# Performance work log

Measured on AMD Instinct MI355X. Metric: run time of the kernel, lower is better.

## Reference

```python
import math
import jax, jax.numpy as jnp
import numpy as np

B, N, DQ, DK, DV, H = 8, 1024, 256, 256, 256, 8
EPS_SM = 1e-15
EPS_LN = 1e-5


def _layer_norm(x, g, b):
    mu = jnp.mean(x, axis=-1, keepdims=True)
    var = jnp.mean((x - mu) ** 2, axis=-1, keepdims=True)
    return (x - mu) * jax.lax.rsqrt(var + EPS_LN) * g + b


def setup_inputs() -> dict:
    key = jax.random.key(0)
    ks = jax.random.split(key, 16)
    s = 0.05
    inp = {
        "Q": jax.random.normal(ks[0], (B, N, DQ), jnp.float32),
        "K": jax.random.normal(ks[1], (B, N, DK), jnp.float32),
        "lengths": jnp.clip(jax.random.randint(ks[2], (B,), 0, N), 1, N),
        "Wq": jax.random.normal(ks[3], (DQ, DV), jnp.float32) * s,
        "bq": jnp.zeros((DV,), jnp.float32),
        "Wk": jax.random.normal(ks[4], (DK, DV), jnp.float32) * s,
        "bk": jnp.zeros((DV,), jnp.float32),
        "Wv": jax.random.normal(ks[5], (DK, DV), jnp.float32) * s,
        "bv": jnp.zeros((DV,), jnp.float32),
        "Wo": jax.random.normal(ks[6], (DV, DV), jnp.float32) * s,
        "bo": jnp.zeros((DV,), jnp.float32),
        "g0": jnp.ones((DV,), jnp.float32),
        "b0": jnp.zeros((DV,), jnp.float32),
        "g1": jnp.ones((DV,), jnp.float32),
        "b1": jnp.zeros((DV,), jnp.float32),
    }
    return inp


def reference(Q, K, lengths, Wq, bq, Wk, bk, Wv, bv, Wo, bo, g0, b0, g1, b1):
    d = DV // H  # head dim
    mask = (jnp.arange(N) < lengths[:, None]).astype(Q.dtype)  # (B, N)
    q = (Q @ Wq + bq) * mask[..., None]  # (B, N, DV)
    k = (K @ Wk + bk) * mask[..., None]
    v = (K @ Wv + bv) * mask[..., None]
    qh = q.reshape(B, N, H, d)
    kh = k.reshape(B, N, H, d)
    vh = v.reshape(B, N, H, d)
    # NB: original scales by sqrt(dim_V), not sqrt(head_dim)
    scores = jnp.einsum("bnhd,bmhd->bhnm", qh, kh) / math.sqrt(DV)
    # set_softmax: raw exp, mask rows and cols by lengths, normalize over keys
    e = jnp.exp(scores) * mask[:, None, :, None] * mask[:, None, None, :]
    A = e / (jnp.sum(e, axis=-1, keepdims=True) + EPS_SM)  # (B, H, N, N)
    O = qh + jnp.einsum("bhnm,bmhd->bnhd", A, vh)  # residual per head
    O = O.reshape(B, N, DV)
    O = _layer_norm(O, g0, b0)
    O = O + jax.nn.relu(O @ Wo + bo)
    O = _layer_norm(O, g1, b1)
    return O
```

## Files before the change

kernel.cpp:

```cpp
#include <hip/hip_runtime.h>
#include <hip/hip_bf16.h>


typedef __attribute__((ext_vector_type(8))) short short8;
typedef __attribute__((ext_vector_type(4))) short short4v;
typedef __attribute__((ext_vector_type(4))) float f32x4;

__device__ __forceinline__ short f2bf(float f) {
    union { float f; unsigned u; } x; x.f = f;
    unsigned r = x.u + 0x7fffu + ((x.u >> 16) & 1u);
    return (short)(r >> 16);
}
__device__ __forceinline__ float bf2f(short s) {
    union { unsigned u; float f; } x; x.u = ((unsigned)(unsigned short)s) << 16;
    return x.f;
}

__global__ __launch_bounds__(256) void wtrans_kernel(
    const float* __restrict__ Wq, const float* __restrict__ Wk,
    const float* __restrict__ Wv, const float* __restrict__ Wo,
    short* __restrict__ WqT, short* __restrict__ WkT,
    short* __restrict__ WvT, short* __restrict__ WoT)
{
    __shared__ short tile[64][72];
    const float* W; short* T;
    switch (blockIdx.y) {
        case 0:  W = Wq; T = WqT; break;
        case 1:  W = Wk; T = WkT; break;
        case 2:  W = Wv; T = WvT; break;
        default: W = Wo; T = WoT; break;
    }
    const int k0 = (blockIdx.x >> 2) * 64;
    const int n0 = (blockIdx.x & 3) * 64;
    const int c  = threadIdx.x & 63;
    const int r4 = threadIdx.x >> 6;
    #pragma unroll
    for (int i = 0; i < 16; i++) {
        int k = r4 + i * 4;
        tile[k][c] = f2bf(W[(size_t)(k0 + k) * 256 + n0 + c]);
    }
    __syncthreads();
    #pragma unroll
    for (int i = 0; i < 16; i++) {
        int n = r4 + i * 4;
        T[(size_t)(n0 + n) * 256 + k0 + c] = tile[c][n];
    }
}

__global__ __launch_bounds__(256) void proj_kernel(
    const float* __restrict__ Q, const float* __restrict__ Kin,
    const short* __restrict__ WqT, const short* __restrict__ WkT, const short* __restrict__ WvT,
    const float* __restrict__ bq, const float* __restrict__ bk, const float* __restrict__ bv,
    const int* __restrict__ lengths,
    short* __restrict__ qb, short* __restrict__ kb, short* __restrict__ vT)
{
    __shared__ short Xt[32][264];
    const int which = blockIdx.y;
    const float* A   = (which == 0) ? Q   : Kin;
    const short* WTa = (which == 0) ? WqT : WkT;

    const int tid = threadIdx.x;
    const int b = blockIdx.x >> 5;
    const int len = lengths[b];
    const int r0b = blockIdx.x * 32;
    const int ntok0b = r0b & 1023;

    if (ntok0b < len) {
        #pragma unroll
        for (int it = 0; it < 8; it++) {
            int e = tid + it * 256;
            int row = e >> 6, c4 = (e & 63) * 4;
            float4 f = *(const float4*)(A + (size_t)(r0b + row) * 256 + c4);
            short4v s4;
            s4[0] = f2bf(f.x); s4[1] = f2bf(f.y); s4[2] = f2bf(f.z); s4[3] = f2bf(f.w);
            *(short4v*)(&Xt[row][c4]) = s4;
        }
    }
    __syncthreads();

    const int lane = tid & 63, wid = tid >> 6;
    const int m = lane & 15, quad = lane >> 4;
    const int rh = wid >> 1, ch = wid & 1;
    const int c0 = ch * 128;
    const int ntok0 = ntok0b + rh * 16;

    f32x4 accA[8], accB[8];
    #pragma unroll
    for (int t = 0; t < 8; t++) {
        accA[t] = (f32x4){0.f, 0.f, 0.f, 0.f};
        accB[t] = (f32x4){0.f, 0.f, 0.f, 0.f};
    }

    if (ntok0 < len) {
        for (int kk = 0; kk < 256; kk += 32) {
            short8 af = *(const short8*)(&Xt[rh * 16 + m][kk + quad * 8]);
            #pragma unroll
            for (int t = 0; t < 8; t++) {
                short8 bfa = *(const short8*)(WTa + (c0 + t * 16 + m) * 256 + kk + quad * 8);
                accA[t] = __builtin_amdgcn_mfma_f32_16x16x32_bf16(af, bfa, accA[t], 0, 0, 0);
            }
            if (which == 1) {
                #pragma unroll
                for (int t = 0; t < 8; t++) {
                    short8 bfb = *(const short8*)(WvT + (c0 + t * 16 + m) * 256 + kk + quad * 8);
                    accB[t] = __builtin_amdgcn_mfma_f32_16x16x32_bf16(af, bfb, accB[t], 0, 0, 0);
                }
            }
        }
    }

    #pragma unroll
    for (int t = 0; t < 8; t++) {
        int n = c0 + t * 16 + m;
        int h = n >> 5, i = n & 31;
        int bh = b * 8 + h;
        if (which == 0) {
            float bias = bq[n];
            #pragma unroll
            for (int reg = 0; reg < 4; reg++) {
                int ntok = ntok0 + quad * 4 + reg;
                float val = (ntok < len) ? (accA[t][reg] + bias) : 0.f;
                qb[((size_t)bh * 1024 + ntok) * 32 + i] = f2bf(val);
            }
        } else {
            float bk_ = bk[n];
            float bv_ = bv[n];
            #pragma unroll
            for (int reg = 0; reg < 4; reg++) {
                int ntok = ntok0 + quad * 4 + reg;
                bool ok = ntok < len;
                float vk = ok ? (accA[t][reg] + bk_) : 0.f;
                float vv = ok ? (accB[t][reg] + bv_) : 0.f;
                kb[((size_t)bh * 1024 + ntok) * 32 + i] = f2bf(vk);
                vT[(size_t)(bh * 32 + i) * 1024 + ntok] = f2bf(vv);
            }
        }
    }
}

__global__ __launch_bounds__(256) void attn_kernel(
    const short* __restrict__ qb, const short* __restrict__ kb, const short* __restrict__ vT,
    const int* __restrict__ lengths, float* __restrict__ O1)
{
    __shared__ short P[4][16][72];
    __shared__ float cbO[2][16][33];
    __shared__ float cbL[2][16];
    const int tid = threadIdx.x;
    const int lane = tid & 63, wid = tid >> 6;
    const int m = lane & 15, quad = lane >> 4;
    const int ks = wid & 1, qh = wid >> 1;
    const int bh = blockIdx.y;
    const int b = bh >> 3, h = bh & 7;
    const int len = lengths[b];
    const int qr0 = blockIdx.x * 32 + qh * 16;

    const short* qbase = qb + (size_t)bh * 1024 * 32;
    const short* kbase = kb + (size_t)bh * 1024 * 32;
    const short* vbase = vT + (size_t)bh * 32 * 1024;

    const short8 qf = *(const short8*)(qbase + (qr0 + m) * 32 + quad * 8);

    f32x4 o0 = (f32x4){0.f, 0.f, 0.f, 0.f};
    f32x4 o1 = (f32x4){0.f, 0.f, 0.f, 0.f};
    float l[4] = {0.f, 0.f, 0.f, 0.f};

    int nch = 0;
    if (qr0 < len) nch = (len + 63) >> 6;
    const int kchunks = (nch + 1 - ks) >> 1;

    for (int ci = 0; ci < kchunks; ci++) {
        int key0 = (ci * 2 + ks) * 64;
        short8 vf0a = *(const short8*)(vbase + (size_t)(m) * 1024      + key0 + quad * 8);
        short8 vf1a = *(const short8*)(vbase + (size_t)(16 + m) * 1024 + key0 + quad * 8);
        short8 vf0b = *(const short8*)(vbase + (size_t)(m) * 1024      + key0 + 32 + quad * 8);
        short8 vf1b = *(const short8*)(vbase + (size_t)(16 + m) * 1024 + key0 + 32 + quad * 8);
        #pragma unroll
        for (int t = 0; t < 4; t++) {
            short8 kf = *(const short8*)(kbase + (key0 + t * 16 + m) * 32 + quad * 8);
            f32x4 s = __builtin_amdgcn_mfma_f32_16x16x32_bf16(qf, kf,
                        (f32x4){0.f, 0.f, 0.f, 0.f}, 0, 0, 0);
            int col = key0 + t * 16 + m;
            bool cm = col < len;
            #pragma unroll
            for (int reg = 0; reg < 4; reg++) {
                float e = cm ? __expf(s[reg] * 0.0625f) : 0.f;
                l[reg] += e;
                P[wid][quad * 4 + reg][t * 16 + m] = f2bf(e);
            }
        }
        asm volatile("s_waitcnt lgkmcnt(0)" ::: "memory");
        short8 pf0 = *(const short8*)(&P[wid][m][quad * 8]);
        short8 pf1 = *(const short8*)(&P[wid][m][32 + quad * 8]);
        o0 = __builtin_amdgcn_mfma_f32_16x16x32_bf16(pf0, vf0a, o0, 0, 0, 0);
        o1 = __builtin_amdgcn_mfma_f32_16x16x32_bf16(pf0, vf1a, o1, 0, 0, 0);
        o0 = __builtin_amdgcn_mfma_f32_16x16x32_bf16(pf1, vf0b, o0, 0, 0, 0);
        o1 = __builtin_amdgcn_mfma_f32_16x16x32_bf16(pf1, vf1b, o1, 0, 0, 0);
    }

    #pragma unroll
    for (int reg = 0; reg < 4; reg++) {
        float s = l[reg];
        s += __shfl_xor(s, 1); s += __shfl_xor(s, 2);
        s += __shfl_xor(s, 4); s += __shfl_xor(s, 8);
        l[reg] = s;
    }

    if (ks == 1) {
        #pragma unroll
        for (int reg = 0; reg < 4; reg++) {
            cbO[qh][quad * 4 + reg][m]      = o0[reg];
            cbO[qh][quad * 4 + reg][16 + m] = o1[reg];
        }
        if (m == 0) {
            #pragma unroll
            for (int reg = 0; reg < 4; reg++) cbL[qh][quad * 4 + reg] = l[reg];
        }
    }
    __syncthreads();
    if (ks == 0) {
        const int hbase = h * 32;
        #pragma unroll
        for (int reg = 0; reg < 4; reg++) {
            int r = quad * 4 + reg;
            o0[reg] += cbO[qh][r][m];
            o1[reg] += cbO[qh][r][16 + m];
            float lt = l[reg] + cbL[qh][r];
            int qrow = qr0 + r;
            float f = (qrow < len) ? 1.f / (lt + 1e-15f) : 0.f;
            size_t obase = ((size_t)(b * 1024 + qrow)) * 256 + hbase;
            float q0 = bf2f(qbase[qrow * 32 + m]);
            float q1 = bf2f(qbase[qrow * 32 + 16 + m]);
            O1[obase + m]      = q0 + o0[reg] * f;
            O1[obase + 16 + m] = q1 + o1[reg] * f;
        }
    }
}

__global__ __launch_bounds__(256) void out_kernel(
    const float* __restrict__ O1, const short* __restrict__ WoT,
    const float* __restrict__ g0, const float* __restrict__ b0,
    const float* __restrict__ bo, const float* __restrict__ g1, const float* __restrict__ b1,
    float* __restrict__ out)
{
    __shared__ short Xs[16][264];
    __shared__ float st[4][2][16];
    const int tid = threadIdx.x;
    const int r0 = blockIdx.x * 16;

    {
        const int lrow  = tid >> 4;
        const int cbase = (tid & 15) * 16;
        const float* rowp = O1 + (size_t)(r0 + lrow) * 256 + cbase;
        float4 a0 = ((const float4*)rowp)[0];
        float4 a1 = ((const float4*)rowp)[1];
        float4 a2 = ((const float4*)rowp)[2];
        float4 a3 = ((const float4*)rowp)[3];
        float s  = a0.x + a0.y + a0.z + a0.w + a1.x + a1.y + a1.z + a1.w
                 + a2.x + a2.y + a2.z + a2.w + a3.x + a3.y + a3.z + a3.w;
        float s2 = a0.x*a0.x + a0.y*a0.y + a0.z*a0.z + a0.w*a0.w
                 + a1.x*a1.x + a1.y*a1.y + a1.z*a1.z + a1.w*a1.w
                 + a2.x*a2.x + a2.y*a2.y + a2.z*a2.z + a2.w*a2.w
                 + a3.x*a3.x + a3.y*a3.y + a3.z*a3.z + a3.w*a3.w;
        s  += __shfl_xor(s, 1);  s  += __shfl_xor(s, 2);
        s  += __shfl_xor(s, 4);  s  += __shfl_xor(s, 8);
        s2 += __shfl_xor(s2, 1); s2 += __shfl_xor(s2, 2);
        s2 += __shfl_xor(s2, 4); s2 += __shfl_xor(s2, 8);
        float mean = s * (1.f / 256.f);
        float var  = s2 * (1.f / 256.f) - mean * mean;
        float rs = rsqrtf(var + 1e-5f);
        float4 g0a = ((const float4*)(g0 + cbase))[0];
        float4 g0b = ((const float4*)(g0 + cbase))[1];
        float4 g0c = ((const float4*)(g0 + cbase))[2];
        float4 g0d = ((const float4*)(g0 + cbase))[3];
        float4 b0a = ((const float4*)(b0 + cbase))[0];
        float4 b0b = ((const float4*)(b0 + cbase))[1];
        float4 b0c = ((const float4*)(b0 + cbase))[2];
        float4 b0d = ((const float4*)(b0 + cbase))[3];
        short8 y0, y1;
        y0[0] = f2bf((a0.x - mean) * rs * g0a.x + b0a.x);
        y0[1] = f2bf((a0.y - mean) * rs * g0a.y + b0a.y);
        y0[2] = f2bf((a0.z - mean) * rs * g0a.z + b0a.z);
        y0[3] = f2bf((a0.w - mean) * rs * g0a.w + b0a.w);
        y0[4] = f2bf((a1.x - mean) * rs * g0b.x + b0b.x);
        y0[5] = f2bf((a1.y - mean) * rs * g0b.y + b0b.y);
        y0[6] = f2bf((a1.z - mean) * rs * g0b.z + b0b.z);
        y0[7] = f2bf((a1.w - mean) * rs * g0b.w + b0b.w);
        y1[0] = f2bf((a2.x - mean) * rs * g0c.x + b0c.x);
        y1[1] = f2bf((a2.y - mean) * rs * g0c.y + b0c.y);
        y1[2] = f2bf((a2.z - mean) * rs * g0c.z + b0c.z);
        y1[3] = f2bf((a2.w - mean) * rs * g0c.w + b0c.w);
        y1[4] = f2bf((a3.x - mean) * rs * g0d.x + b0d.x);
        y1[5] = f2bf((a3.y - mean) * rs * g0d.y + b0d.y);
        y1[6] = f2bf((a3.z - mean) * rs * g0d.z + b0d.z);
        y1[7] = f2bf((a3.w - mean) * rs * g0d.w + b0d.w);
        *(short8*)(&Xs[lrow][cbase])     = y0;
        *(short8*)(&Xs[lrow][cbase + 8]) = y1;
    }
    __syncthreads();

    const int lane = tid & 63, wid = tid >> 6;
    const int m = lane & 15, quad = lane >> 4;
    const int c0 = wid * 64;

    f32x4 acc[4];
    #pragma unroll
    for (int t = 0; t < 4; t++) acc[t] = (f32x4){0.f, 0.f, 0.f, 0.f};

    for (int kk = 0; kk < 256; kk += 32) {
        short8 af = *(const short8*)(&Xs[m][kk + quad * 8]);
        #pragma unroll
        for (int t = 0; t < 4; t++) {
            short8 bf = *(const short8*)(WoT + (c0 + t * 16 + m) * 256 + kk + quad * 8);
            acc[t] = __builtin_amdgcn_mfma_f32_16x16x32_bf16(af, bf, acc[t], 0, 0, 0);
        }
    }

    float s1[4] = {0.f, 0.f, 0.f, 0.f};
    float s2v[4] = {0.f, 0.f, 0.f, 0.f};
    #pragma unroll
    for (int t = 0; t < 4; t++) {
        int n = c0 + t * 16 + m;
        float bon = bo[n];
        #pragma unroll
        for (int reg = 0; reg < 4; reg++) {
            int r = quad * 4 + reg;
            float xv = bf2f(Xs[r][n]);
            float c = acc[t][reg] + bon;
            float yv = xv + (c > 0.f ? c : 0.f);
            acc[t][reg] = yv;
            s1[reg] += yv;
            s2v[reg] += yv * yv;
        }
    }
    #pragma unroll
    for (int reg = 0; reg < 4; reg++) {
        float a = s1[reg], bsum = s2v[reg];
        a += __shfl_xor(a, 1); a += __shfl_xor(a, 2); a += __shfl_xor(a, 4); a += __shfl_xor(a, 8);
        bsum += __shfl_xor(bsum, 1); bsum += __shfl_xor(bsum, 2); bsum += __shfl_xor(bsum, 4); bsum += __shfl_xor(bsum, 8);
        s1[reg] = a; s2v[reg] = bsum;
    }
    if (m == 0) {
        #pragma unroll
        for (int reg = 0; reg < 4; reg++) {
            st[wid][0][quad * 4 + reg] = s1[reg];
            st[wid][1][quad * 4 + reg] = s2v[reg];
        }
    }
    __syncthreads();
    #pragma unroll
    for (int reg = 0; reg < 4; reg++) {
        int r = quad * 4 + reg;
        float t1 = st[0][0][r] + st[1][0][r] + st[2][0][r] + st[3][0][r];
        float t2 = st[0][1][r] + st[1][1][r] + st[2][1][r] + st[3][1][r];
        float mean = t1 * (1.f / 256.f);
        float var  = t2 * (1.f / 256.f) - mean * mean;
        float rs = rsqrtf(var + 1e-5f);
        int token = r0 + r;
        #pragma unroll
        for (int t = 0; t < 4; t++) {
            int n = c0 + t * 16 + m;
            out[(size_t)token * 256 + n] = (acc[t][reg] - mean) * rs * g1[n] + b1[n];
        }
    }
}

extern "C" void kernel_launch(void* const* d_in, const int* in_sizes, int n_in,
                              void* d_out, int out_size, void* d_ws, size_t ws_size,
                              hipStream_t stream) {
    const float* Q   = (const float*)d_in[0];
    const float* K   = (const float*)d_in[1];
    const int* lengths = (const int*)d_in[2];
    const float* Wq  = (const float*)d_in[3];
    const float* bq  = (const float*)d_in[4];
    const float* Wk  = (const float*)d_in[5];
    const float* bk  = (const float*)d_in[6];
    const float* Wv  = (const float*)d_in[7];
    const float* bv  = (const float*)d_in[8];
    const float* Wo  = (const float*)d_in[9];
    const float* bo  = (const float*)d_in[10];
    const float* g0  = (const float*)d_in[11];
    const float* b0  = (const float*)d_in[12];
    const float* g1  = (const float*)d_in[13];
    const float* b1  = (const float*)d_in[14];
    float* out = (float*)d_out;

    char* ws = (char*)d_ws;
    short* qb  = (short*)(ws);
    short* kb  = (short*)(ws + (4u << 20));
    short* vT  = (short*)(ws + (8u << 20));
    float* O1  = (float*)(ws + (12u << 20));
    short* WqT = (short*)(ws + (20u << 20));
    short* WkT = (short*)(ws + (20u << 20) + (128u << 10));
    short* WvT = (short*)(ws + (20u << 20) + (256u << 10));
    short* WoT = (short*)(ws + (20u << 20) + (384u << 10));

    wtrans_kernel<<<dim3(16, 4), 256, 0, stream>>>(Wq, Wk, Wv, Wo, WqT, WkT, WvT, WoT);
    proj_kernel<<<dim3(256, 2), 256, 0, stream>>>(Q, K, WqT, WkT, WvT, bq, bk, bv,
                                                  lengths, qb, kb, vT);
    attn_kernel<<<dim3(32, 64), 256, 0, stream>>>(qb, kb, vT, lengths, O1);
    out_kernel<<<dim3(512), 256, 0, stream>>>(O1, WoT, g0, b0, bo, g1, b1, out);
}
```

Baseline: 157.0 us.

## Stage K/V tiles in shared memory across four query waves with register prefetch

The attention kernel now assigns 64 query rows per block, one 16-row slab per wave. Each 64-key K/V chunk is loaded cooperatively into double-buffered LDS with a register prefetch of the next chunk, replacing per-wave global loads and the split-key cross-wave reduction. The 1/16 score scale is folded into K in the projection kernel, which removes a multiply per exp but changes bf16 rounding of K slightly. The cost is one block barrier per chunk, and inactive waves still have to join every barrier.

```diff
diff --git a/kernel.cpp b/kernel.cpp
--- a/kernel.cpp
+++ b/kernel.cpp
@@ -109,6 +109,7 @@
         }
     }
 
+    const float KSCALE = 0.0625f;
     #pragma unroll
     for (int t = 0; t < 8; t++) {
         int n = c0 + t * 16 + m;
@@ -129,7 +130,7 @@
             for (int reg = 0; reg < 4; reg++) {
                 int ntok = ntok0 + quad * 4 + reg;
                 bool ok = ntok < len;
-                float vk = ok ? (accA[t][reg] + bk_) : 0.f;
+                float vk = ok ? (accA[t][reg] + bk_) * KSCALE : 0.f;
                 float vv = ok ? (accB[t][reg] + bv_) : 0.f;
                 kb[((size_t)bh * 1024 + ntok) * 32 + i] = f2bf(vk);
                 vT[(size_t)(bh * 32 + i) * 1024 + ntok] = f2bf(vv);
@@ -142,17 +143,17 @@
     const short* __restrict__ qb, const short* __restrict__ kb, const short* __restrict__ vT,
     const int* __restrict__ lengths, float* __restrict__ O1)
 {
+    __shared__ short Kb[2][64][36];
+    __shared__ short Vb[2][32][76];
     __shared__ short P[4][16][72];
-    __shared__ float cbO[2][16][33];
-    __shared__ float cbL[2][16];
     const int tid = threadIdx.x;
     const int lane = tid & 63, wid = tid >> 6;
     const int m = lane & 15, quad = lane >> 4;
-    const int ks = wid & 1, qh = wid >> 1;
     const int bh = blockIdx.y;
     const int b = bh >> 3, h = bh & 7;
     const int len = lengths[b];
-    const int qr0 = blockIdx.x * 32 + qh * 16;
+    const int qr0 = blockIdx.x * 64 + wid * 16;
+    const bool active = qr0 < len;
 
     const short* qbase = qb + (size_t)bh * 1024 * 32;
     const short* kbase = kb + (size_t)bh * 1024 * 32;
@@ -164,37 +165,51 @@
     f32x4 o1 = (f32x4){0.f, 0.f, 0.f, 0.f};
     float l[4] = {0.f, 0.f, 0.f, 0.f};
 
-    int nch = 0;
-    if (qr0 < len) nch = (len + 63) >> 6;
-    const int kchunks = (nch + 1 - ks) >> 1;
-
-    for (int ci = 0; ci < kchunks; ci++) {
-        int key0 = (ci * 2 + ks) * 64;
-        short8 vf0a = *(const short8*)(vbase + (size_t)(m) * 1024      + key0 + quad * 8);
-        short8 vf1a = *(const short8*)(vbase + (size_t)(16 + m) * 1024 + key0 + quad * 8);
-        short8 vf0b = *(const short8*)(vbase + (size_t)(m) * 1024      + key0 + 32 + quad * 8);
-        short8 vf1b = *(const short8*)(vbase + (size_t)(16 + m) * 1024 + key0 + 32 + quad * 8);
-        #pragma unroll
-        for (int t = 0; t < 4; t++) {
-            short8 kf = *(const short8*)(kbase + (key0 + t * 16 + m) * 32 + quad * 8);
-            f32x4 s = __builtin_amdgcn_mfma_f32_16x16x32_bf16(qf, kf,
-                        (f32x4){0.f, 0.f, 0.f, 0.f}, 0, 0, 0);
-            int col = key0 + t * 16 + m;
-            bool cm = col < len;
-            #pragma unroll
-            for (int reg = 0; reg < 4; reg++) {
-                float e = cm ? __expf(s[reg] * 0.0625f) : 0.f;
-                l[reg] += e;
-                P[wid][quad * 4 + reg][t * 16 + m] = f2bf(e);
-            }
-        }
-        asm volatile("s_waitcnt lgkmcnt(0)" ::: "memory");
-        short8 pf0 = *(const short8*)(&P[wid][m][quad * 8]);
-        short8 pf1 = *(const short8*)(&P[wid][m][32 + quad * 8]);
-        o0 = __builtin_amdgcn_mfma_f32_16x16x32_bf16(pf0, vf0a, o0, 0, 0, 0);
-        o1 = __builtin_amdgcn_mfma_f32_16x16x32_bf16(pf0, vf1a, o1, 0, 0, 0);
-        o0 = __builtin_amdgcn_mfma_f32_16x16x32_bf16(pf1, vf0b, o0, 0, 0, 0);
-        o1 = __builtin_amdgcn_mfma_f32_16x16x32_bf16(pf1, vf1b, o1, 0, 0, 0);
+    const int nch = (blockIdx.x * 64 < len) ? ((len + 63) >> 6) : 0;
+
+    short8 kr, vr;
+    if (nch > 0) {
+        kr = *(const short8*)(kbase + tid * 8);
+        vr = *(const short8*)(vbase + (size_t)(tid >> 3) * 1024 + (tid & 7) * 8);
+    }
+
+    for (int ci = 0; ci < nch; ci++) {
+        const int buf = ci & 1;
+        *(short8*)(&Kb[buf][tid >> 2][(tid & 3) * 8]) = kr;
+        *(short8*)(&Vb[buf][tid >> 3][(tid & 7) * 8]) = vr;
+        if (ci + 1 < nch) {
+            int k1 = (ci + 1) * 64;
+            kr = *(const short8*)(kbase + k1 * 32 + tid * 8);
+            vr = *(const short8*)(vbase + (size_t)(tid >> 3) * 1024 + k1 + (tid & 7) * 8);
+        }
+        __syncthreads();
+
+        if (active) {
+            const int key0 = ci * 64;
+            #pragma unroll
+            for (int t = 0; t < 4; t++) {
+                short8 kf = *(const short8*)(&Kb[buf][t * 16 + m][quad * 8]);
+                f32x4 s = __builtin_amdgcn_mfma_f32_16x16x32_bf16(qf, kf,
+                            (f32x4){0.f, 0.f, 0.f, 0.f}, 0, 0, 0);
+                int col = key0 + t * 16 + m;
+                bool cm = col < len;
+                #pragma unroll
+                for (int reg = 0; reg < 4; reg++) {
+                    float e = cm ? __expf(s[reg]) : 0.f;
+                    l[reg] += e;
+                    P[wid][quad * 4 + reg][t * 16 + m] = f2bf(e);
+                }
+            }
+            asm volatile("s_waitcnt lgkmcnt(0)" ::: "memory");
+            #pragma unroll
+            for (int c = 0; c < 2; c++) {
+                short8 pf  = *(const short8*)(&P[wid][m][c * 32 + quad * 8]);
+                short8 vf0 = *(const short8*)(&Vb[buf][m][c * 32 + quad * 8]);
+                short8 vf1 = *(const short8*)(&Vb[buf][16 + m][c * 32 + quad * 8]);
+                o0 = __builtin_amdgcn_mfma_f32_16x16x32_bf16(pf, vf0, o0, 0, 0, 0);
+                o1 = __builtin_amdgcn_mfma_f32_16x16x32_bf16(pf, vf1, o1, 0, 0, 0);
+            }
+        }
     }
 
     #pragma unroll
@@ -205,34 +220,16 @@
         l[reg] = s;
     }
 
-    if (ks == 1) {
-        #pragma unroll
-        for (int reg = 0; reg < 4; reg++) {
-            cbO[qh][quad * 4 + reg][m]      = o0[reg];
-            cbO[qh][quad * 4 + reg][16 + m] = o1[reg];
-        }
-        if (m == 0) {
-            #pragma unroll
-            for (int reg = 0; reg < 4; reg++) cbL[qh][quad * 4 + reg] = l[reg];
-        }
-    }
-    __syncthreads();
-    if (ks == 0) {
-        const int hbase = h * 32;
-        #pragma unroll
-        for (int reg = 0; reg < 4; reg++) {
-            int r = quad * 4 + reg;
-            o0[reg] += cbO[qh][r][m];
-            o1[reg] += cbO[qh][r][16 + m];
-            float lt = l[reg] + cbL[qh][r];
-            int qrow = qr0 + r;
-            float f = (qrow < len) ? 1.f / (lt + 1e-15f) : 0.f;
-            size_t obase = ((size_t)(b * 1024 + qrow)) * 256 + hbase;
-            float q0 = bf2f(qbase[qrow * 32 + m]);
-            float q1 = bf2f(qbase[qrow * 32 + 16 + m]);
-            O1[obase + m]      = q0 + o0[reg] * f;
-            O1[obase + 16 + m] = q1 + o1[reg] * f;
-        }
+    const int hbase = h * 32;
+    #pragma unroll
+    for (int reg = 0; reg < 4; reg++) {
+        int qrow = qr0 + quad * 4 + reg;
+        float f = (qrow < len) ? 1.f / (l[reg] + 1e-15f) : 0.f;
+        size_t obase = ((size_t)(b * 1024 + qrow)) * 256 + hbase;
+        float q0 = bf2f(qbase[qrow * 32 + m]);
+        float q1 = bf2f(qbase[qrow * 32 + 16 + m]);
+        O1[obase + m]      = q0 + o0[reg] * f;
+        O1[obase + 16 + m] = q1 + o1[reg] * f;
     }
 }
 
@@ -397,6 +394,6 @@
     wtrans_kernel<<<dim3(16, 4), 256, 0, stream>>>(Wq, Wk, Wv, Wo, WqT, WkT, WvT, WoT);
     proj_kernel<<<dim3(256, 2), 256, 0, stream>>>(Q, K, WqT, WkT, WvT, bq, bk, bv,
                                                   lengths, qb, kb, vT);
-    attn_kernel<<<dim3(32, 64), 256, 0, stream>>>(qb, kb, vT, lengths, O1);
+    attn_kernel<<<dim3(16, 64), 256, 0, stream>>>(qb, kb, vT, lengths, O1);
     out_kernel<<<dim3(512), 256, 0, stream>>>(O1, WoT, g0, b0, bo, g1, b1, out);
 }
```

New measurement: 150.7 us (median of 2 runs). 4.0% less time.
